# Optimization experiments

Hardware: AMD Instinct MI355X
Metric: run time of the kernel (lower is better)

The kernel has to match this reference:

```python
import jax, jax.numpy as jnp
import numpy as np

TOKENS, D_IN, D_OUT, RANK = 16384, 4096, 4096, 512

def setup_inputs() -> dict:
    key = jax.random.key(0)
    k1, k2, k3, k4 = jax.random.split(key, 4)
    x = jax.random.normal(k1, (TOKENS, D_IN), dtype=jnp.float32)
    U = jax.random.normal(k2, (D_OUT, RANK), dtype=jnp.float32) * 0.02
    sigma = jax.random.uniform(k3, (RANK,), dtype=jnp.float32)
    V = jax.random.normal(k4, (D_IN, RANK), dtype=jnp.float32) * 0.02
    return {"x": x, "U": U, "sigma": sigma, "V": V}

def reference(x, U, sigma, V):
    # W = U @ diag(sigma) @ V.T  (shape [out, in]); out = x @ W.T
    # diag(sigma) contraction expressed as a column scale of U (same math).
    W = (U * sigma[None, :]) @ V.T          # [out, in]
    return x @ W.T                          # [tokens, out]
```

## Files before the change

kernel.cpp:

```cpp
#include <hip/hip_runtime.h>

typedef __bf16 bf16;
typedef __bf16 bf16x4 __attribute__((ext_vector_type(4)));
typedef __bf16 bf16x8 __attribute__((ext_vector_type(8)));
typedef float  f32x4  __attribute__((ext_vector_type(4)));

#define TOKENS 16384
#define D_IN   4096
#define D_OUT  4096
#define RANK   512

__device__ inline void gload_lds16(const void* g, void* l) {
    __builtin_amdgcn_global_load_lds((const __attribute__((address_space(1))) void*)g,
                                     (__attribute__((address_space(3))) void*)l,
                                     16, 0, 0);
}

__global__ __launch_bounds__(256) void vt_scale(const float* __restrict__ V,
                                                const float* __restrict__ sg,
                                                bf16* __restrict__ Vst) {
    __shared__ float tile[64][65];
    const int tx = threadIdx.x & 63;
    const int ty = threadIdx.x >> 6;
    const int kb = blockIdx.x * 64;
    const int rb = blockIdx.y * 64;
    const float s = sg[rb + tx];
#pragma unroll
    for (int i = ty; i < 64; i += 4)
        tile[i][tx] = V[(size_t)(kb + i) * RANK + rb + tx] * s;
    __syncthreads();
#pragma unroll
    for (int i = ty; i < 64; i += 4) {
        int r = rb + i;
        int kp = kb + (tx ^ ((r & 7) << 3));
        Vst[(size_t)r * D_IN + kp] = (bf16)tile[tx][i];
    }
}

__global__ __launch_bounds__(256) void cvt_bf16_4(const float* __restrict__ in,
                                                  bf16* __restrict__ o, int n4) {
    int i = blockIdx.x * 256 + threadIdx.x;
    if (i < n4) {
        f32x4 v = *(const f32x4*)(in + (size_t)i * 4);
        bf16x4 b = { (bf16)v[0], (bf16)v[1], (bf16)v[2], (bf16)v[3] };
        *(bf16x4*)(o + (size_t)i * 4) = b;
    }
}

__device__ inline bf16x8 cvt8(f32x4 a, f32x4 b) {
    bf16x8 r;
    r[0] = (bf16)a[0]; r[1] = (bf16)a[1]; r[2] = (bf16)a[2]; r[3] = (bf16)a[3];
    r[4] = (bf16)b[0]; r[5] = (bf16)b[1]; r[6] = (bf16)b[2]; r[7] = (bf16)b[3];
    return r;
}

__global__ __launch_bounds__(256) void gemm1_alds(const float* __restrict__ A,
                                                  const bf16* __restrict__ B,
                                                  bf16* __restrict__ T,
                                                  int M, int N, int K) {
    __shared__ float Afl[128 * 64];
    __shared__ bf16  Bl[128 * 64];

    const int t  = threadIdx.x;
    const int l  = t & 63;
    const int w  = t >> 6;
    const int wr = w >> 1, wc = w & 1;
    const int lr = l & 15;
    const int kg = l >> 4;
    const int sxorB = (lr & 7) << 3;

    const int nwg = gridDim.x;
    const int bid = blockIdx.x;
    const int cpx = nwg >> 3;
    const int swz = (bid & 7) * cpx + (bid >> 3);
    const int ntn = N >> 7;
    const int tm  = (swz / ntn) << 7;
    const int tn  = (swz % ntn) << 7;

    const int arow = t >> 4;
    const int acr  = t & 15;
    const float* Asrc = A + (size_t)(tm + arow) * K + ((acr ^ arow) << 2);
    const bf16* Bp = B + (size_t)(tn + (t >> 3)) * K + (t & 7) * 8;

    f32x4 acc[4][4] = {};

    for (int kt = 0; kt < K; kt += 64) {
#pragma unroll
        for (int c = 0; c < 8; ++c)
            gload_lds16(Asrc + kt + (size_t)(c * 16) * K, &Afl[(c * 256 + t) * 4]);
#pragma unroll
        for (int c = 0; c < 4; ++c)
            gload_lds16(Bp + kt + (size_t)(c * 32) * K, &Bl[(c * 256 + t) * 8]);
        __syncthreads();

#pragma unroll
        for (int ks = 0; ks < 2; ++ks) {
            bf16x8 af[4], bfr[4];
            const int q0 = ks * 8 + kg * 2;
#pragma unroll
            for (int f = 0; f < 4; ++f) {
                const float* Arow = &Afl[(wr * 64 + f * 16 + lr) * 64];
                f32x4 h0 = *(const f32x4*)&Arow[(q0 ^ lr) << 2];
                f32x4 h1 = *(const f32x4*)&Arow[((q0 + 1) ^ lr) << 2];
                af[f] = cvt8(h0, h1);
                bfr[f] = *(const bf16x8*)&Bl[(wc * 64 + f * 16 + lr) * 64 +
                                             ((ks * 32 + kg * 8) ^ sxorB)];
            }
#pragma unroll
            for (int fm = 0; fm < 4; ++fm)
#pragma unroll
                for (int fn = 0; fn < 4; ++fn)
                    acc[fm][fn] = __builtin_amdgcn_mfma_f32_16x16x32_bf16(
                        af[fm], bfr[fn], acc[fm][fn], 0, 0, 0);
        }
        __syncthreads();
    }

    const int r0 = tm + wr * 64 + kg * 4;
    const int c0 = tn + wc * 64 + lr;
#pragma unroll
    for (int fm = 0; fm < 4; ++fm)
#pragma unroll
        for (int fn = 0; fn < 4; ++fn)
#pragma unroll
            for (int r = 0; r < 4; ++r)
                T[(size_t)(r0 + fm * 16 + r) * N + (c0 + fn * 16)] = (bf16)acc[fm][fn][r];
}

__global__ __launch_bounds__(256) void gemm2_bt(const bf16* __restrict__ A,
                                                const bf16* __restrict__ B,
                                                float* __restrict__ out,
                                                int M, int N, int K) {
    __shared__ bf16 Al[128 * 64];
    __shared__ bf16 Bl[128 * 64];

    const int t  = threadIdx.x;
    const int l  = t & 63;
    const int w  = t >> 6;
    const int wr = w >> 1, wc = w & 1;
    const int lr = l & 15;
    const int kg = l >> 4;

    const int nwg = gridDim.x;
    const int bid = blockIdx.x;
    const int cpx = nwg >> 3;
    const int swz = (bid & 7) * cpx + (bid >> 3);
    const int ntn = N >> 7;
    const int tm  = (swz / ntn) << 7;
    const int tn  = (swz % ntn) << 7;

    f32x4 acc[4][4] = {};

    for (int kt = 0; kt < K; kt += 64) {
#pragma unroll
        for (int c = 0; c < 4; ++c) {
            int i = c * 256 + t;
            gload_lds16(A + (size_t)(tm + (i >> 3)) * K + kt + (i & 7) * 8, &Al[i * 8]);
        }
#pragma unroll
        for (int c = 0; c < 4; ++c) {
            int i = c * 256 + t;
            gload_lds16(B + (size_t)(tn + (i >> 3)) * K + kt + (i & 7) * 8, &Bl[i * 8]);
        }
        __syncthreads();

#pragma unroll
        for (int ks = 0; ks < 2; ++ks) {
            bf16x8 af[4], bfr[4];
#pragma unroll
            for (int f = 0; f < 4; ++f) {
                af[f]  = *(const bf16x8*)&Al[(wr * 64 + f * 16 + lr) * 64 + ks * 32 + kg * 8];
                bfr[f] = *(const bf16x8*)&Bl[(wc * 64 + f * 16 + lr) * 64 + ks * 32 + kg * 8];
            }
#pragma unroll
            for (int fm = 0; fm < 4; ++fm)
#pragma unroll
                for (int fn = 0; fn < 4; ++fn)
                    acc[fm][fn] = __builtin_amdgcn_mfma_f32_16x16x32_bf16(
                        af[fm], bfr[fn], acc[fm][fn], 0, 0, 0);
        }
        __syncthreads();
    }

    const int r0 = tm + wr * 64 + kg * 4;
    const int c0 = tn + wc * 64 + lr;
#pragma unroll
    for (int fm = 0; fm < 4; ++fm)
#pragma unroll
        for (int fn = 0; fn < 4; ++fn)
#pragma unroll
            for (int r = 0; r < 4; ++r)
                out[(size_t)(r0 + fm * 16 + r) * N + (c0 + fn * 16)] = acc[fm][fn][r];
}

extern "C" void kernel_launch(void* const* d_in, const int* in_sizes, int n_in,
                              void* d_out, int out_size, void* d_ws, size_t ws_size,
                              hipStream_t stream) {
    const float* x  = (const float*)d_in[0];
    const float* U  = (const float*)d_in[1];
    const float* sg = (const float*)d_in[2];
    const float* V  = (const float*)d_in[3];
    float* out = (float*)d_out;

    char* ws = (char*)d_ws;
    bf16* Vst = (bf16*)ws;
    bf16* Ub  = (bf16*)(ws + (4u << 20));
    bf16* T   = (bf16*)(ws + (8u << 20));

    vt_scale<<<dim3(D_IN / 64, RANK / 64), 256, 0, stream>>>(V, sg, Vst);
    cvt_bf16_4<<<(D_OUT * RANK / 4 + 255) / 256, 256, 0, stream>>>(U, Ub, D_OUT * RANK / 4);

    gemm1_alds<<<(TOKENS / 128) * (RANK / 128), 256, 0, stream>>>(
        x, Vst, T, TOKENS, RANK, D_IN);

    gemm2_bt<<<(TOKENS / 128) * (D_OUT / 128), 256, 0, stream>>>(
        T, Ub, out, TOKENS, D_OUT, RANK);
}
```

Baseline: 264.6 us.

## Rewrite second GEMM with 256x256 double-buffered tiles and swizzled LDS layout

Replaces the 128x128 single-buffered second GEMM with a 512-thread, 256x256-tile kernel that double-buffers LDS via async global-to-LDS loads, uses explicit vmcnt waits, barriers and MFMA priority hints. The intermediate T and the converted U are now written in an XOR-swizzled layout so LDS fragment reads avoid bank conflicts. It targets the LDS bank conflicts, load latency and low arithmetic intensity of the dominant 16384x4096x512 GEMM. It raises register and LDS pressure (128 KB LDS per block), which may limit occupancy.

```diff
diff --git a/kernel.cpp b/kernel.cpp
--- a/kernel.cpp
+++ b/kernel.cpp
@@ -37,14 +37,19 @@
     }
 }
 
-__global__ __launch_bounds__(256) void cvt_bf16_4(const float* __restrict__ in,
-                                                  bf16* __restrict__ o, int n4) {
-    int i = blockIdx.x * 256 + threadIdx.x;
-    if (i < n4) {
-        f32x4 v = *(const f32x4*)(in + (size_t)i * 4);
-        bf16x4 b = { (bf16)v[0], (bf16)v[1], (bf16)v[2], (bf16)v[3] };
-        *(bf16x4*)(o + (size_t)i * 4) = b;
-    }
+__global__ __launch_bounds__(256) void cvt_u_swz(const float* __restrict__ U,
+                                                 bf16* __restrict__ Ub) {
+    int g = blockIdx.x * 256 + threadIdx.x;
+    int n = g >> 6;
+    int c = g & 63;
+    int blk = c >> 3, q = c & 7;
+    const float* src = U + (size_t)n * RANK + c * 8;
+    f32x4 v0 = *(const f32x4*)src;
+    f32x4 v1 = *(const f32x4*)(src + 4);
+    bf16x8 b;
+    b[0] = (bf16)v0[0]; b[1] = (bf16)v0[1]; b[2] = (bf16)v0[2]; b[3] = (bf16)v0[3];
+    b[4] = (bf16)v1[0]; b[5] = (bf16)v1[1]; b[6] = (bf16)v1[2]; b[7] = (bf16)v1[3];
+    *(bf16x8*)(Ub + (size_t)n * RANK + blk * 64 + ((q ^ (n & 7)) * 8)) = b;
 }
 
 __device__ inline bf16x8 cvt8(f32x4 a, f32x4 b) {
@@ -123,74 +128,117 @@
 #pragma unroll
         for (int fn = 0; fn < 4; ++fn)
 #pragma unroll
-            for (int r = 0; r < 4; ++r)
-                T[(size_t)(r0 + fm * 16 + r) * N + (c0 + fn * 16)] = (bf16)acc[fm][fn][r];
-}
-
-__global__ __launch_bounds__(256) void gemm2_bt(const bf16* __restrict__ A,
-                                                const bf16* __restrict__ B,
-                                                float* __restrict__ out,
-                                                int M, int N, int K) {
-    __shared__ bf16 Al[128 * 64];
-    __shared__ bf16 Bl[128 * 64];
-
-    const int t  = threadIdx.x;
-    const int l  = t & 63;
-    const int w  = t >> 6;
-    const int wr = w >> 1, wc = w & 1;
-    const int lr = l & 15;
-    const int kg = l >> 4;
+            for (int r = 0; r < 4; ++r) {
+                int row = r0 + fm * 16 + r;
+                int col = (c0 + fn * 16) ^ ((row & 7) << 3);
+                T[(size_t)row * N + col] = (bf16)acc[fm][fn][r];
+            }
+}
+
+__global__ __launch_bounds__(512, 2) void gemm2_8p(const bf16* __restrict__ A,
+                                                   const bf16* __restrict__ B,
+                                                   float* __restrict__ out,
+                                                   int M, int N, int K) {
+    __shared__ bf16 Al[2][256 * 64];
+    __shared__ bf16 Bl[2][256 * 64];
+
+    const int t   = threadIdx.x;
+    const int l   = t & 63;
+    const int wid = t >> 6;
+    const int wm  = wid >> 2;
+    const int wn  = wid & 3;
+    const int lr  = l & 15;
+    const int kg  = l >> 4;
+    const int sxor = (lr & 7) << 3;
 
     const int nwg = gridDim.x;
     const int bid = blockIdx.x;
     const int cpx = nwg >> 3;
     const int swz = (bid & 7) * cpx + (bid >> 3);
-    const int ntn = N >> 7;
-    const int tm  = (swz / ntn) << 7;
-    const int tn  = (swz % ntn) << 7;
-
-    f32x4 acc[4][4] = {};
-
-    for (int kt = 0; kt < K; kt += 64) {
-#pragma unroll
-        for (int c = 0; c < 4; ++c) {
-            int i = c * 256 + t;
-            gload_lds16(A + (size_t)(tm + (i >> 3)) * K + kt + (i & 7) * 8, &Al[i * 8]);
+    const int ntn = N >> 8;
+    const int tm  = (swz / ntn) << 8;
+    const int tn  = (swz % ntn) << 8;
+
+    const bf16* Apt = A + (size_t)(tm + (t >> 3)) * K + (t & 7) * 8;
+    const bf16* Bpt = B + (size_t)(tn + (t >> 3)) * K + (t & 7) * 8;
+    const int ldst = t * 8;
+
+    const int NT = K >> 6;
+
+    f32x4 acc[8][4] = {};
+    bf16x8 aq[4][2], bq[2][2];
+
+#define STAGE(BUF, KT)                                                         \
+    _Pragma("unroll") for (int c = 0; c < 4; ++c) {                            \
+        gload_lds16(Apt + (KT) + (size_t)(c * 64) * K, &Al[BUF][c * 4096 + ldst]); \
+        gload_lds16(Bpt + (KT) + (size_t)(c * 64) * K, &Bl[BUF][c * 4096 + ldst]); \
+    }
+
+#define RD_A(BUF, QM)                                                          \
+    _Pragma("unroll") for (int f = 0; f < 4; ++f)                              \
+    _Pragma("unroll") for (int ks = 0; ks < 2; ++ks)                           \
+        aq[f][ks] = *(const bf16x8*)&Al[BUF][(wm * 128 + (QM) * 64 + f * 16 + lr) * 64 + \
+                                            ((ks * 32 + kg * 8) ^ sxor)];
+
+#define RD_B(BUF, QN)                                                          \
+    _Pragma("unroll") for (int f = 0; f < 2; ++f)                              \
+    _Pragma("unroll") for (int ks = 0; ks < 2; ++ks)                           \
+        bq[f][ks] = *(const bf16x8*)&Bl[BUF][(wn * 64 + (QN) * 32 + f * 16 + lr) * 64 + \
+                                            ((ks * 32 + kg * 8) ^ sxor)];
+
+#define MM(QM, QN)                                                             \
+    __builtin_amdgcn_s_setprio(1);                                             \
+    _Pragma("unroll") for (int ks = 0; ks < 2; ++ks)                           \
+    _Pragma("unroll") for (int fm = 0; fm < 4; ++fm)                           \
+    _Pragma("unroll") for (int fn = 0; fn < 2; ++fn)                           \
+        acc[(QM) * 4 + fm][(QN) * 2 + fn] = __builtin_amdgcn_mfma_f32_16x16x32_bf16( \
+            aq[fm][ks], bq[fn][ks], acc[(QM) * 4 + fm][(QN) * 2 + fn], 0, 0, 0); \
+    __builtin_amdgcn_s_setprio(0);
+
+    STAGE(0, 0);
+    STAGE(1, 64);
+    asm volatile("s_waitcnt vmcnt(8)" ::: "memory");
+    __builtin_amdgcn_sched_barrier(0);
+    __builtin_amdgcn_s_barrier();
+    __builtin_amdgcn_sched_barrier(0);
+
+    for (int i = 0; i < NT; ++i) {
+        const int p = i & 1;
+        RD_A(p, 0); RD_B(p, 0); MM(0, 0);
+        RD_B(p, 1);             MM(0, 1);
+        RD_A(p, 1); RD_B(p, 0); MM(1, 0);
+        RD_B(p, 1);             MM(1, 1);
+
+        if (i + 1 < NT) {
+            __builtin_amdgcn_sched_barrier(0);
+            __builtin_amdgcn_s_barrier();
+            __builtin_amdgcn_sched_barrier(0);
+            if (i + 2 < NT) {
+                STAGE(p, (i + 2) * 64);
+                asm volatile("s_waitcnt vmcnt(8)" ::: "memory");
+            } else {
+                asm volatile("s_waitcnt vmcnt(0)" ::: "memory");
+            }
+            __builtin_amdgcn_sched_barrier(0);
+            __builtin_amdgcn_s_barrier();
+            __builtin_amdgcn_sched_barrier(0);
         }
-#pragma unroll
-        for (int c = 0; c < 4; ++c) {
-            int i = c * 256 + t;
-            gload_lds16(B + (size_t)(tn + (i >> 3)) * K + kt + (i & 7) * 8, &Bl[i * 8]);
-        }
-        __syncthreads();
-
-#pragma unroll
-        for (int ks = 0; ks < 2; ++ks) {
-            bf16x8 af[4], bfr[4];
-#pragma unroll
-            for (int f = 0; f < 4; ++f) {
-                af[f]  = *(const bf16x8*)&Al[(wr * 64 + f * 16 + lr) * 64 + ks * 32 + kg * 8];
-                bfr[f] = *(const bf16x8*)&Bl[(wc * 64 + f * 16 + lr) * 64 + ks * 32 + kg * 8];
-            }
-#pragma unroll
-            for (int fm = 0; fm < 4; ++fm)
-#pragma unroll
-                for (int fn = 0; fn < 4; ++fn)
-                    acc[fm][fn] = __builtin_amdgcn_mfma_f32_16x16x32_bf16(
-                        af[fm], bfr[fn], acc[fm][fn], 0, 0, 0);
-        }
-        __syncthreads();
-    }
-
-    const int r0 = tm + wr * 64 + kg * 4;
-    const int c0 = tn + wc * 64 + lr;
-#pragma unroll
-    for (int fm = 0; fm < 4; ++fm)
+    }
+
+    const int r0 = tm + wm * 128 + kg * 4;
+    const int c0 = tn + wn * 64 + lr;
+#pragma unroll
+    for (int fm = 0; fm < 8; ++fm)
 #pragma unroll
         for (int fn = 0; fn < 4; ++fn)
 #pragma unroll
             for (int r = 0; r < 4; ++r)
                 out[(size_t)(r0 + fm * 16 + r) * N + (c0 + fn * 16)] = acc[fm][fn][r];
+
+#undef STAGE
+#undef RD_A
+#undef RD_B
+#undef MM
 }
 
 extern "C" void kernel_launch(void* const* d_in, const int* in_sizes, int n_in,
@@ -208,11 +256,11 @@
     bf16* T   = (bf16*)(ws + (8u << 20));
 
     vt_scale<<<dim3(D_IN / 64, RANK / 64), 256, 0, stream>>>(V, sg, Vst);
-    cvt_bf16_4<<<(D_OUT * RANK / 4 + 255) / 256, 256, 0, stream>>>(U, Ub, D_OUT * RANK / 4);
+    cvt_u_swz<<<(D_OUT * RANK / 8) / 256, 256, 0, stream>>>(U, Ub);
 
     gemm1_alds<<<(TOKENS / 128) * (RANK / 128), 256, 0, stream>>>(
         x, Vst, T, TOKENS, RANK, D_IN);
 
-    gemm2_bt<<<(TOKENS / 128) * (D_OUT / 128), 256, 0, stream>>>(
+    gemm2_8p<<<(TOKENS / 256) * (D_OUT / 256), 512, 0, stream>>>(
         T, Ub, out, TOKENS, D_OUT, RANK);
 }
```

After: 250.8 us, median of 2. 1.05x faster.
